# Performance work log

Hardware: AMD Instinct MI355X
Metric: run time of the kernel (lower is better)

The kernel has to match this reference:

```python
import jax, jax.numpy as jnp
import numpy as np

ALPHA = 0.2  # LeakyReLU negative slope


def setup_inputs() -> dict:
    key = jax.random.key(0)
    k1, k2, k3, k4 = jax.random.split(key, 4)
    B, N, in_dim, out_dim, n_heads = 4, 2048, 128, 32, 4
    H = jax.random.normal(k1, (B, N, in_dim), dtype=jnp.float32)
    adj = jax.random.randint(k2, (N, N), 0, 2).astype(jnp.float32)
    # xavier-uniform-like init for params
    limW = np.sqrt(6.0 / (in_dim + out_dim))
    W = jax.random.uniform(k3, (n_heads, in_dim, out_dim), minval=-limW, maxval=limW, dtype=jnp.float32)
    lima = np.sqrt(6.0 / (n_heads + 2 * out_dim))
    a = jax.random.uniform(k4, (n_heads, 2 * out_dim), minval=-lima, maxval=lima, dtype=jnp.float32)
    return {"H": H, "adj": adj, "W": W, "a": a}


def reference(H, adj, W, a):
    B, N, _ = H.shape
    n_heads, _, out_dim = W.shape
    # projected features: (B, H, N, F)
    Ht = jnp.einsum('bni,hio->bhno', H, W)
    # split attention vector: e_ij = leaky_relu(a_src . h_i + a_dst . h_j)
    a_src, a_dst = a[:, :out_dim], a[:, out_dim:]
    src = jnp.einsum('bhnf,hf->bhn', Ht, a_src)  # (B,H,N)
    dst = jnp.einsum('bhnf,hf->bhn', Ht, a_dst)  # (B,H,N)
    e = src[:, :, :, None] + dst[:, :, None, :]  # (B,H,N,N)
    e = jnp.where(e >= 0, e, ALPHA * e)          # leaky_relu
    mask = (adj + jnp.eye(N, dtype=adj.dtype)) != 0  # (N,N) bool, self-loops added
    e = jnp.where(mask[None, None], e, -jnp.inf)
    alpha = jax.nn.softmax(e, axis=-1)           # (B,H,N,N)
    H_new = jnp.einsum('bhnj,bhjf->bhnf', alpha, Ht)
    H_new = jnp.where(H_new > 0, H_new, jnp.expm1(H_new))  # ELU
    # concat heads: (B, N, n_heads*out_dim)
    H_new = jnp.transpose(H_new, (0, 2, 1, 3)).reshape(B, N, n_heads * out_dim)
    return H_new, alpha
```

## Files before the change

kernel.cpp:

```cpp
#include <hip/hip_runtime.h>
#include <hip/hip_bf16.h>
#include <math.h>


typedef float f32x4 __attribute__((ext_vector_type(4)));
typedef short bf16x8 __attribute__((ext_vector_type(8)));
typedef unsigned int u32;

#define LRELU 0.2f
#define LOG2E 1.44269504088896f
#define EXP2(x) __builtin_amdgcn_exp2f(x)

__device__ inline ushort f2b(float x) {
    unsigned int u = __float_as_uint(x);
    u += 0x7fffu + ((u >> 16) & 1u);
    return (ushort)(u >> 16);
}

__global__ __launch_bounds__(256) void k01(const float* __restrict__ adj,
                                           unsigned char* __restrict__ adjI,
                                           const float* __restrict__ H,
                                           const float* __restrict__ W,
                                           const float* __restrict__ a,
                                           __hip_bfloat16* __restrict__ HtT,
                                           float* __restrict__ src,
                                           float* __restrict__ dst) {
    __shared__ __align__(16) ushort Wbf[32 * 128];

    int bid = blockIdx.x;
    int t = threadIdx.x;

    if (bid >= 512) {
        int idx = (bid - 512) * 256 + t;
        int e0 = idx * 4;
        int row = e0 >> 11;
        int c0 = e0 & 2047;
        float4 v = *(const float4*)(adj + (size_t)e0);
        uchar4 o;
        o.x = (v.x != 0.f || c0     == row) ? 1 : 0;
        o.y = (v.y != 0.f || c0 + 1 == row) ? 1 : 0;
        o.z = (v.z != 0.f || c0 + 2 == row) ? 1 : 0;
        o.w = (v.w != 0.f || c0 + 3 == row) ? 1 : 0;
        *(uchar4*)(adjI + (size_t)e0) = o;
        return;
    }

    int ntile = bid & 31;
    int bh = bid >> 5;
    int b = bh >> 2, h = bh & 3;
    int lane = t & 63, w = t >> 6;
    int l15 = lane & 15, l4 = lane >> 4;

    #pragma unroll
    for (int u = 0; u < 16; ++u) {
        int idx = u * 256 + t;
        int i = idx >> 5, f = idx & 31;
        Wbf[(f * 128 + i) ^ ((f & 7) << 3)] = f2b(W[h * 4096 + idx]);
    }
    __syncthreads();

    int n = ntile * 64 + w * 16 + l15;
    const float* hrow = H + ((size_t)(b * 2048) + n) * 128;

    f32x4 acc0 = {0.f, 0.f, 0.f, 0.f};
    f32x4 acc1 = {0.f, 0.f, 0.f, 0.f};
    #pragma unroll
    for (int kc = 0; kc < 4; ++kc) {
        int k0 = kc * 32 + l4 * 8;
        float4 h0 = *(const float4*)(hrow + k0);
        float4 h1 = *(const float4*)(hrow + k0 + 4);
        union { u32 u[4]; bf16x8 v; } bu;
        asm("v_cvt_pk_bf16_f32 %0, %1, %2" : "=v"(bu.u[0]) : "v"(h0.x), "v"(h0.y));
        asm("v_cvt_pk_bf16_f32 %0, %1, %2" : "=v"(bu.u[1]) : "v"(h0.z), "v"(h0.w));
        asm("v_cvt_pk_bf16_f32 %0, %1, %2" : "=v"(bu.u[2]) : "v"(h1.x), "v"(h1.y));
        asm("v_cvt_pk_bf16_f32 %0, %1, %2" : "=v"(bu.u[3]) : "v"(h1.z), "v"(h1.w));
        bf16x8 bfrag = bu.v;
        bf16x8 af0 = *(const bf16x8*)&Wbf[(l15 * 128 + kc * 32 + l4 * 8) ^ ((l15 & 7) << 3)];
        bf16x8 af1 = *(const bf16x8*)&Wbf[((16 + l15) * 128 + kc * 32 + l4 * 8) ^ (((16 + l15) & 7) << 3)];
        acc0 = __builtin_amdgcn_mfma_f32_16x16x32_bf16(af0, bfrag, acc0, 0, 0, 0);
        acc1 = __builtin_amdgcn_mfma_f32_16x16x32_bf16(af1, bfrag, acc1, 0, 0, 0);
    }

    float sv = 0.f, dvv = 0.f;
    #pragma unroll
    for (int r = 0; r < 4; ++r) {
        int f0 = l4 * 4 + r;
        sv  += acc0[r] * a[h * 64 + f0]      + acc1[r] * a[h * 64 + 16 + f0];
        dvv += acc0[r] * a[h * 64 + 32 + f0] + acc1[r] * a[h * 64 + 48 + f0];
    }
    sv  += __shfl_xor(sv, 16);  sv  += __shfl_xor(sv, 32);
    dvv += __shfl_xor(dvv, 16); dvv += __shfl_xor(dvv, 32);
    if (l4 == 0) { src[bh * 2048 + n] = sv; dst[bh * 2048 + n] = dvv; }

    __syncthreads();
    ushort* T = Wbf;
    int nl = w * 16 + l15;
    #pragma unroll
    for (int r = 0; r < 4; ++r) {
        int f0 = l4 * 4 + r;
        T[f0 * 64 + nl]        = f2b(acc0[r]);
        T[(16 + f0) * 64 + nl] = f2b(acc1[r]);
    }
    __syncthreads();
    {
        int f = t >> 3, n8 = (t & 7) * 8;
        uint4 v = *(const uint4*)&T[f * 64 + n8];
        *(uint4*)((ushort*)HtT + (size_t)(bh * 32 + f) * 2048 + ntile * 64 + n8) = v;
    }
}

__global__ __launch_bounds__(256, 4) void k2_fused(const unsigned char* __restrict__ adjI,
                                                   const float* __restrict__ src,
                                                   const float* __restrict__ dst,
                                                   const __hip_bfloat16* __restrict__ HtT,
                                                   float* __restrict__ alpha,
                                                   float* __restrict__ outH) {
    __shared__ float dstS[2048];
    __shared__ float rowL[32], rowSrcS[32];
    __shared__ __align__(16) ushort As[2][32 * 128];

    int t = threadIdx.x;
    int mtile = blockIdx.x;
    int bh    = blockIdx.y;
    int lane = t & 63, w = t >> 6;
    int b = bh >> 2, h = bh & 3;
    int row0 = mtile * 32;

    const float4* dst4g = (const float4*)(dst + bh * 2048);
    #pragma unroll
    for (int u = 0; u < 2; ++u) {
        float4 v = dst4g[u * 256 + t];
        v.x *= LOG2E; v.y *= LOG2E; v.z *= LOG2E; v.w *= LOG2E;
        *(float4*)&dstS[(u * 256 + t) * 4] = v;
    }
    if (t < 32) rowSrcS[t] = src[bh * 2048 + row0 + t] * LOG2E;
    __syncthreads();

    for (int rr = 0; rr < 8; ++rr) {
        int r = w * 8 + rr;
        int gr = row0 + r;
        float sn = rowSrcS[r];
        const uint4* a16 = (const uint4*)(adjI + (size_t)gr * 2048);
        float S = 0.f;
        #pragma unroll
        for (int u = 0; u < 2; ++u) {
            uint4 ab = a16[u * 64 + lane];
            int jb = (u * 64 + lane) * 16;
            u32 words[4] = {ab.x, ab.y, ab.z, ab.w};
            #pragma unroll
            for (int wq = 0; wq < 4; ++wq) {
                float4 dv = *(const float4*)&dstS[jb + wq * 4];
                float dj[4] = {dv.x, dv.y, dv.z, dv.w};
                #pragma unroll
                for (int q = 0; q < 4; ++q) {
                    float ajf = (float)((words[wq] >> (8 * q)) & 0xffu);
                    float ee = sn + dj[q];
                    float vm = fmaxf(ee, LRELU * ee);
                    S = fmaf(EXP2(vm), ajf, S);
                }
            }
        }
        #pragma unroll
        for (int off = 32; off; off >>= 1) S += __shfl_xor(S, off);
        if (lane == 0) rowL[r] = -__log2f(S);
    }
    __syncthreads();

    f32x4 acc = {0.f, 0.f, 0.f, 0.f};
    int wr = w >> 1, wc = w & 1;
    int l15 = lane & 15, l4 = lane >> 4;
    int arow = wr * 16 + l15;
    const ushort* Bfp = (const ushort*)HtT + (size_t)(bh * 32 + wc * 16 + l15) * 2048 + l4 * 8;
    float* alphaRow = alpha + (size_t)(bh * 2048 + row0) * 2048;

    int sr = t >> 5;
    int sc4 = t & 31;

    float snR[4], LR[4];
    #pragma unroll
    for (int u = 0; u < 4; ++u) { snR[u] = rowSrcS[sr + u * 8]; LR[u] = rowL[sr + u * 8]; }

    auto loadA = [&](int k, u32* ar) {
        #pragma unroll
        for (int u = 0; u < 4; ++u)
            ar[u] = *(const u32*)(adjI + (size_t)(row0 + sr + u * 8) * 2048 + k * 128 + sc4 * 4);
    };
    auto loadB = [&](int k, bf16x8* br) {
        #pragma unroll
        for (int kk = 0; kk < 4; ++kk)
            br[kk] = *(const bf16x8*)(Bfp + (size_t)k * 128 + kk * 32);
    };
    auto stage = [&](int k, const u32* ar, ushort* Asb) {
        int jb = k * 128 + sc4 * 4;
        float4 dv = *(const float4*)&dstS[jb];
        float dj[4] = {dv.x, dv.y, dv.z, dv.w};
        #pragma unroll
        for (int u = 0; u < 4; ++u) {
            int r = sr + u * 8;
            float sn = snR[u], L = LR[u];
            u32 ab = ar[u];
            float o[4];
            #pragma unroll
            for (int q = 0; q < 4; ++q) {
                float ajf = (float)((ab >> (8 * q)) & 0xffu);
                float ee = sn + dj[q];
                float vm = fmaxf(ee + L, fmaf(ee, LRELU, L));
                o[q] = EXP2(vm) * ajf;
            }
            f32x4 ov = {o[0], o[1], o[2], o[3]};
            *(f32x4*)(alphaRow + (size_t)r * 2048 + jb) = ov;
            u32 lo, hi;
            asm("v_cvt_pk_bf16_f32 %0, %1, %2" : "=v"(lo) : "v"(o[0]), "v"(o[1]));
            asm("v_cvt_pk_bf16_f32 %0, %1, %2" : "=v"(hi) : "v"(o[2]), "v"(o[3]));
            uint2 pk = {lo, hi};
            *(uint2*)&Asb[(r * 128 + sc4 * 4) ^ ((r & 7) << 3)] = pk;
        }
    };
    auto mfmaPhase = [&](const bf16x8* br, const ushort* Asb) {
        #pragma unroll
        for (int kk = 0; kk < 4; ++kk) {
            bf16x8 af = *(const bf16x8*)&Asb[(arow * 128 + kk * 32 + l4 * 8) ^ ((arow & 7) << 3)];
            acc = __builtin_amdgcn_mfma_f32_16x16x32_bf16(af, br[kk], acc, 0, 0, 0);
        }
    };

    u32 aE[4], aO[4];
    bf16x8 bE[4], bO[4];
    loadA(0, aE); loadB(0, bE);

    for (int kp = 0; kp < 8; ++kp) {
        int ke = 2 * kp, ko = 2 * kp + 1;
        loadA(ko, aO); loadB(ko, bO);
        __builtin_amdgcn_sched_barrier(0);
        stage(ke, aE, As[0]);
        asm volatile("s_waitcnt lgkmcnt(0)" ::: "memory");
        __builtin_amdgcn_s_barrier();
        mfmaPhase(bE, As[0]);
        if (ko + 1 < 16) { loadA(ko + 1, aE); loadB(ko + 1, bE); }
        __builtin_amdgcn_sched_barrier(0);
        stage(ko, aO, As[1]);
        asm volatile("s_waitcnt lgkmcnt(0)" ::: "memory");
        __builtin_amdgcn_s_barrier();
        mfmaPhase(bO, As[1]);
    }

    #pragma unroll
    for (int q = 0; q < 4; ++q) {
        int node = row0 + wr * 16 + l4 * 4 + q;
        float v = acc[q];
        v = (v > 0.f) ? v : expm1f(v);
        outH[(size_t)(b * 2048 + node) * 128 + h * 32 + wc * 16 + l15] = v;
    }
}

extern "C" void kernel_launch(void* const* d_in, const int* in_sizes, int n_in,
                              void* d_out, int out_size, void* d_ws, size_t ws_size,
                              hipStream_t stream) {
    const float* H   = (const float*)d_in[0];
    const float* adj = (const float*)d_in[1];
    const float* W   = (const float*)d_in[2];
    const float* a   = (const float*)d_in[3];

    float* outH  = (float*)d_out;
    float* alpha = outH + (size_t)4 * 2048 * 128;

    char* ws = (char*)d_ws;
    __hip_bfloat16* HtT = (__hip_bfloat16*)ws;
    float* src = (float*)(ws + 2 * 1024 * 1024);
    float* dst = src + 32768;
    unsigned char* adjI = (unsigned char*)(ws + 2 * 1024 * 1024 + 256 * 1024);

    k01<<<4608, 256, 0, stream>>>(adj, adjI, H, W, a, HtT, src, dst);
    k2_fused<<<dim3(64, 16), 256, 0, stream>>>(adjI, src, dst, HtT, alpha, outH);
}
```

Baseline: 71.25 us.

## Stage half-row alpha tiles into large LDS buffer, cutting barriers per tile

The k2 main loop now works on two halves of 1024 columns instead of sixteen 128-column chunks. Each wave computes full 1024-wide alpha rows for its own 8 rows, writes them to global memory and to a 64KB bf16 LDS buffer, then syncs once before running all the MFMAs for that half. This is meant to cut the number of block barriers and to make the global alpha stores contiguous per row. In exchange, LDS use rises to roughly 72KB per block, so launch bounds drop from 4 to 2 blocks per CU and occupancy falls. Compute and MFMA phases also no longer overlap across chunks.

```diff
diff --git a/kernel.cpp b/kernel.cpp
--- a/kernel.cpp
+++ b/kernel.cpp
@@ -109,7 +109,7 @@
     }
 }
 
-__global__ __launch_bounds__(256, 4) void k2_fused(const unsigned char* __restrict__ adjI,
+__global__ __launch_bounds__(256, 2) void k2_fused(const unsigned char* __restrict__ adjI,
                                                    const float* __restrict__ src,
                                                    const float* __restrict__ dst,
                                                    const __hip_bfloat16* __restrict__ HtT,
@@ -117,7 +117,7 @@
                                                    float* __restrict__ outH) {
     __shared__ float dstS[2048];
     __shared__ float rowL[32], rowSrcS[32];
-    __shared__ __align__(16) ushort As[2][32 * 128];
+    __shared__ __align__(16) ushort As[32 * 1024];
 
     int t = threadIdx.x;
     int mtile = blockIdx.x;
@@ -173,75 +173,79 @@
     const ushort* Bfp = (const ushort*)HtT + (size_t)(bh * 32 + wc * 16 + l15) * 2048 + l4 * 8;
     float* alphaRow = alpha + (size_t)(bh * 2048 + row0) * 2048;
 
-    int sr = t >> 5;
-    int sc4 = t & 31;
-
-    float snR[4], LR[4];
-    #pragma unroll
-    for (int u = 0; u < 4; ++u) { snR[u] = rowSrcS[sr + u * 8]; LR[u] = rowL[sr + u * 8]; }
-
-    auto loadA = [&](int k, u32* ar) {
-        #pragma unroll
-        for (int u = 0; u < 4; ++u)
-            ar[u] = *(const u32*)(adjI + (size_t)(row0 + sr + u * 8) * 2048 + k * 128 + sc4 * 4);
-    };
-    auto loadB = [&](int k, bf16x8* br) {
+    #pragma unroll
+    for (int half = 0; half < 2; ++half) {
+        int c0 = half * 1024;
+
+        u32 abE[4], abO[4];
+        {
+            const u32* ap = (const u32*)(adjI + (size_t)(row0 + w * 8) * 2048 + c0);
+            #pragma unroll
+            for (int j = 0; j < 4; ++j) abE[j] = ap[j * 64 + lane];
+        }
+        #pragma unroll
+        for (int rr = 0; rr < 8; ++rr) {
+            int r = w * 8 + rr;
+            const u32* abC = (rr & 1) ? abO : abE;
+            u32*       abN = (rr & 1) ? abE : abO;
+            if (rr < 7) {
+                const u32* ap = (const u32*)(adjI + (size_t)(row0 + r + 1) * 2048 + c0);
+                #pragma unroll
+                for (int j = 0; j < 4; ++j) abN[j] = ap[j * 64 + lane];
+            }
+            __builtin_amdgcn_sched_barrier(0);
+            float sn = rowSrcS[r], L = rowL[r];
+            float* orow = alphaRow + (size_t)r * 2048 + c0;
+            #pragma unroll
+            for (int j = 0; j < 4; ++j) {
+                int col = j * 256 + lane * 4;
+                float4 dv = *(const float4*)&dstS[c0 + col];
+                float dj[4] = {dv.x, dv.y, dv.z, dv.w};
+                u32 ab = abC[j];
+                float o[4];
+                #pragma unroll
+                for (int q = 0; q < 4; ++q) {
+                    float ajf = (float)((ab >> (8 * q)) & 0xffu);
+                    float ee = sn + dj[q];
+                    float vm = fmaxf(ee + L, fmaf(ee, LRELU, L));
+                    o[q] = EXP2(vm) * ajf;
+                }
+                f32x4 ov = {o[0], o[1], o[2], o[3]};
+                *(f32x4*)(orow + col) = ov;
+                u32 lo, hi;
+                asm("v_cvt_pk_bf16_f32 %0, %1, %2" : "=v"(lo) : "v"(o[0]), "v"(o[1]));
+                asm("v_cvt_pk_bf16_f32 %0, %1, %2" : "=v"(hi) : "v"(o[2]), "v"(o[3]));
+                uint2 pk = {lo, hi};
+                *(uint2*)&As[(r * 1024 + col) ^ ((r & 7) << 3)] = pk;
+            }
+        }
+
+        bf16x8 bE[4], bO[4];
         #pragma unroll
         for (int kk = 0; kk < 4; ++kk)
-            br[kk] = *(const bf16x8*)(Bfp + (size_t)k * 128 + kk * 32);
-    };
-    auto stage = [&](int k, const u32* ar, ushort* Asb) {
-        int jb = k * 128 + sc4 * 4;
-        float4 dv = *(const float4*)&dstS[jb];
-        float dj[4] = {dv.x, dv.y, dv.z, dv.w};
-        #pragma unroll
-        for (int u = 0; u < 4; ++u) {
-            int r = sr + u * 8;
-            float sn = snR[u], L = LR[u];
-            u32 ab = ar[u];
-            float o[4];
-            #pragma unroll
-            for (int q = 0; q < 4; ++q) {
-                float ajf = (float)((ab >> (8 * q)) & 0xffu);
-                float ee = sn + dj[q];
-                float vm = fmaxf(ee + L, fmaf(ee, LRELU, L));
-                o[q] = EXP2(vm) * ajf;
-            }
-            f32x4 ov = {o[0], o[1], o[2], o[3]};
-            *(f32x4*)(alphaRow + (size_t)r * 2048 + jb) = ov;
-            u32 lo, hi;
-            asm("v_cvt_pk_bf16_f32 %0, %1, %2" : "=v"(lo) : "v"(o[0]), "v"(o[1]));
-            asm("v_cvt_pk_bf16_f32 %0, %1, %2" : "=v"(hi) : "v"(o[2]), "v"(o[3]));
-            uint2 pk = {lo, hi};
-            *(uint2*)&Asb[(r * 128 + sc4 * 4) ^ ((r & 7) << 3)] = pk;
-        }
-    };
-    auto mfmaPhase = [&](const bf16x8* br, const ushort* Asb) {
-        #pragma unroll
-        for (int kk = 0; kk < 4; ++kk) {
-            bf16x8 af = *(const bf16x8*)&Asb[(arow * 128 + kk * 32 + l4 * 8) ^ ((arow & 7) << 3)];
-            acc = __builtin_amdgcn_mfma_f32_16x16x32_bf16(af, br[kk], acc, 0, 0, 0);
-        }
-    };
-
-    u32 aE[4], aO[4];
-    bf16x8 bE[4], bO[4];
-    loadA(0, aE); loadB(0, bE);
-
-    for (int kp = 0; kp < 8; ++kp) {
-        int ke = 2 * kp, ko = 2 * kp + 1;
-        loadA(ko, aO); loadB(ko, bO);
-        __builtin_amdgcn_sched_barrier(0);
-        stage(ke, aE, As[0]);
+            bE[kk] = *(const bf16x8*)(Bfp + (size_t)(half * 8) * 128 + kk * 32);
         asm volatile("s_waitcnt lgkmcnt(0)" ::: "memory");
         __builtin_amdgcn_s_barrier();
-        mfmaPhase(bE, As[0]);
-        if (ko + 1 < 16) { loadA(ko + 1, aE); loadB(ko + 1, bE); }
-        __builtin_amdgcn_sched_barrier(0);
-        stage(ko, aO, As[1]);
+
+        #pragma unroll
+        for (int c = 0; c < 8; ++c) {
+            const bf16x8* bC = (c & 1) ? bO : bE;
+            bf16x8*       bN = (c & 1) ? bE : bO;
+            if (c < 7) {
+                #pragma unroll
+                for (int kk = 0; kk < 4; ++kk)
+                    bN[kk] = *(const bf16x8*)(Bfp + (size_t)(half * 8 + c + 1) * 128 + kk * 32);
+            }
+            __builtin_amdgcn_sched_barrier(0);
+            #pragma unroll
+            for (int kk = 0; kk < 4; ++kk) {
+                bf16x8 af = *(const bf16x8*)&As[(arow * 1024 + c * 128 + kk * 32 + l4 * 8) ^ ((arow & 7) << 3)];
+                acc = __builtin_amdgcn_mfma_f32_16x16x32_bf16(af, bC[kk], acc, 0, 0, 0);
+            }
+        }
+
         asm volatile("s_waitcnt lgkmcnt(0)" ::: "memory");
         __builtin_amdgcn_s_barrier();
-        mfmaPhase(bO, As[1]);
     }
 
     #pragma unroll
```

After: 84.34 us. +18.4%, slower.

## Restructure fused attention kernel to single-wave blocks of 16 rows without barriers

Applied to the files above, without the earlier changes.

The fused softmax/aggregation kernel moves from 256-thread blocks over 32 rows to 64-thread single-wavefront blocks over 16 rows, doubling the grid. With one wave per block, all __syncthreads and s_barrier calls are dropped. Each wave now computes both 16-column output halves with two MFMA accumulators and loads B fragments inline per chunk. This removes cross-wave synchronisation but reloads the 8KB dst vector into LDS per 16 rows (twice as often) and gives each wave more serial work and register pressure.

```diff
diff --git a/kernel.cpp b/kernel.cpp
--- a/kernel.cpp
+++ b/kernel.cpp
@@ -109,37 +109,36 @@
     }
 }
 
-__global__ __launch_bounds__(256, 4) void k2_fused(const unsigned char* __restrict__ adjI,
-                                                   const float* __restrict__ src,
-                                                   const float* __restrict__ dst,
-                                                   const __hip_bfloat16* __restrict__ HtT,
-                                                   float* __restrict__ alpha,
-                                                   float* __restrict__ outH) {
+__global__ __launch_bounds__(64, 2) void k2_fused(const unsigned char* __restrict__ adjI,
+                                                  const float* __restrict__ src,
+                                                  const float* __restrict__ dst,
+                                                  const __hip_bfloat16* __restrict__ HtT,
+                                                  float* __restrict__ alpha,
+                                                  float* __restrict__ outH) {
     __shared__ float dstS[2048];
-    __shared__ float rowL[32], rowSrcS[32];
-    __shared__ __align__(16) ushort As[2][32 * 128];
-
-    int t = threadIdx.x;
+    __shared__ float rowL[16], rowSrc[16];
+    __shared__ __align__(16) ushort As[2][16 * 128];
+
+    int lane = threadIdx.x;
     int mtile = blockIdx.x;
     int bh    = blockIdx.y;
-    int lane = t & 63, w = t >> 6;
     int b = bh >> 2, h = bh & 3;
-    int row0 = mtile * 32;
+    int row0 = mtile * 16;
+    int l15 = lane & 15, l4 = lane >> 4;
 
     const float4* dst4g = (const float4*)(dst + bh * 2048);
     #pragma unroll
-    for (int u = 0; u < 2; ++u) {
-        float4 v = dst4g[u * 256 + t];
+    for (int u = 0; u < 8; ++u) {
+        float4 v = dst4g[u * 64 + lane];
         v.x *= LOG2E; v.y *= LOG2E; v.z *= LOG2E; v.w *= LOG2E;
-        *(float4*)&dstS[(u * 256 + t) * 4] = v;
-    }
-    if (t < 32) rowSrcS[t] = src[bh * 2048 + row0 + t] * LOG2E;
-    __syncthreads();
-
-    for (int rr = 0; rr < 8; ++rr) {
-        int r = w * 8 + rr;
+        *(float4*)&dstS[(u * 64 + lane) * 4] = v;
+    }
+    if (lane < 16) rowSrc[lane] = src[bh * 2048 + row0 + lane] * LOG2E;
+
+    #pragma unroll
+    for (int r = 0; r < 16; ++r) {
         int gr = row0 + r;
-        float sn = rowSrcS[r];
+        float sn = rowSrc[r];
         const uint4* a16 = (const uint4*)(adjI + (size_t)gr * 2048);
         float S = 0.f;
         #pragma unroll
@@ -164,41 +163,33 @@
         for (int off = 32; off; off >>= 1) S += __shfl_xor(S, off);
         if (lane == 0) rowL[r] = -__log2f(S);
     }
-    __syncthreads();
-
-    f32x4 acc = {0.f, 0.f, 0.f, 0.f};
-    int wr = w >> 1, wc = w & 1;
-    int l15 = lane & 15, l4 = lane >> 4;
-    int arow = wr * 16 + l15;
-    const ushort* Bfp = (const ushort*)HtT + (size_t)(bh * 32 + wc * 16 + l15) * 2048 + l4 * 8;
+
+    int r2 = lane >> 5;
+    float snP[8], LP[8];
+    #pragma unroll
+    for (int p = 0; p < 8; ++p) { snP[p] = rowSrc[2 * p + r2]; LP[p] = rowL[2 * p + r2]; }
+
+    f32x4 acc0 = {0.f, 0.f, 0.f, 0.f};
+    f32x4 acc1 = {0.f, 0.f, 0.f, 0.f};
+    const ushort* Bf0 = (const ushort*)HtT + (size_t)(bh * 32 + l15) * 2048 + l4 * 8;
+    const ushort* Bf1 = (const ushort*)HtT + (size_t)(bh * 32 + 16 + l15) * 2048 + l4 * 8;
     float* alphaRow = alpha + (size_t)(bh * 2048 + row0) * 2048;
-
-    int sr = t >> 5;
-    int sc4 = t & 31;
-
-    float snR[4], LR[4];
-    #pragma unroll
-    for (int u = 0; u < 4; ++u) { snR[u] = rowSrcS[sr + u * 8]; LR[u] = rowL[sr + u * 8]; }
+    int sc = (lane & 31) * 4;
 
     auto loadA = [&](int k, u32* ar) {
         #pragma unroll
-        for (int u = 0; u < 4; ++u)
-            ar[u] = *(const u32*)(adjI + (size_t)(row0 + sr + u * 8) * 2048 + k * 128 + sc4 * 4);
-    };
-    auto loadB = [&](int k, bf16x8* br) {
-        #pragma unroll
-        for (int kk = 0; kk < 4; ++kk)
-            br[kk] = *(const bf16x8*)(Bfp + (size_t)k * 128 + kk * 32);
+        for (int p = 0; p < 8; ++p)
+            ar[p] = *(const u32*)(adjI + (size_t)(row0 + 2 * p + r2) * 2048 + k * 128 + sc);
     };
     auto stage = [&](int k, const u32* ar, ushort* Asb) {
-        int jb = k * 128 + sc4 * 4;
+        int jb = k * 128 + sc;
         float4 dv = *(const float4*)&dstS[jb];
         float dj[4] = {dv.x, dv.y, dv.z, dv.w};
         #pragma unroll
-        for (int u = 0; u < 4; ++u) {
-            int r = sr + u * 8;
-            float sn = snR[u], L = LR[u];
-            u32 ab = ar[u];
+        for (int p = 0; p < 8; ++p) {
+            int r = 2 * p + r2;
+            float sn = snP[p], L = LP[p];
+            u32 ab = ar[p];
             float o[4];
             #pragma unroll
             for (int q = 0; q < 4; ++q) {
@@ -213,43 +204,47 @@
             asm("v_cvt_pk_bf16_f32 %0, %1, %2" : "=v"(lo) : "v"(o[0]), "v"(o[1]));
             asm("v_cvt_pk_bf16_f32 %0, %1, %2" : "=v"(hi) : "v"(o[2]), "v"(o[3]));
             uint2 pk = {lo, hi};
-            *(uint2*)&Asb[(r * 128 + sc4 * 4) ^ ((r & 7) << 3)] = pk;
+            *(uint2*)&Asb[(r * 128 + sc) ^ ((r & 7) << 3)] = pk;
         }
     };
-    auto mfmaPhase = [&](const bf16x8* br, const ushort* Asb) {
+    auto chunk = [&](int k, const u32* aC, u32* aN, ushort* Asb) {
+        bf16x8 bf[8];
         #pragma unroll
         for (int kk = 0; kk < 4; ++kk) {
-            bf16x8 af = *(const bf16x8*)&Asb[(arow * 128 + kk * 32 + l4 * 8) ^ ((arow & 7) << 3)];
-            acc = __builtin_amdgcn_mfma_f32_16x16x32_bf16(af, br[kk], acc, 0, 0, 0);
+            bf[kk]     = *(const bf16x8*)(Bf0 + (size_t)k * 128 + kk * 32);
+            bf[4 + kk] = *(const bf16x8*)(Bf1 + (size_t)k * 128 + kk * 32);
+        }
+        if (k < 15) loadA(k + 1, aN);
+        __builtin_amdgcn_sched_barrier(0);
+        stage(k, aC, Asb);
+        bf16x8 af[4];
+        #pragma unroll
+        for (int kk = 0; kk < 4; ++kk)
+            af[kk] = *(const bf16x8*)&Asb[(l15 * 128 + kk * 32 + l4 * 8) ^ ((l15 & 7) << 3)];
+        #pragma unroll
+        for (int kk = 0; kk < 4; ++kk) {
+            acc0 = __builtin_amdgcn_mfma_f32_16x16x32_bf16(af[kk], bf[kk], acc0, 0, 0, 0);
+            acc1 = __builtin_amdgcn_mfma_f32_16x16x32_bf16(af[kk], bf[4 + kk], acc1, 0, 0, 0);
         }
     };
 
-    u32 aE[4], aO[4];
-    bf16x8 bE[4], bO[4];
-    loadA(0, aE); loadB(0, bE);
-
+    u32 aE[8], aO[8];
+    loadA(0, aE);
+    #pragma unroll
     for (int kp = 0; kp < 8; ++kp) {
-        int ke = 2 * kp, ko = 2 * kp + 1;
-        loadA(ko, aO); loadB(ko, bO);
-        __builtin_amdgcn_sched_barrier(0);
-        stage(ke, aE, As[0]);
-        asm volatile("s_waitcnt lgkmcnt(0)" ::: "memory");
-        __builtin_amdgcn_s_barrier();
-        mfmaPhase(bE, As[0]);
-        if (ko + 1 < 16) { loadA(ko + 1, aE); loadB(ko + 1, bE); }
-        __builtin_amdgcn_sched_barrier(0);
-        stage(ko, aO, As[1]);
-        asm volatile("s_waitcnt lgkmcnt(0)" ::: "memory");
-        __builtin_amdgcn_s_barrier();
-        mfmaPhase(bO, As[1]);
+        chunk(2 * kp,     aE, aO, As[0]);
+        chunk(2 * kp + 1, aO, aE, As[1]);
     }
 
     #pragma unroll
     for (int q = 0; q < 4; ++q) {
-        int node = row0 + wr * 16 + l4 * 4 + q;
-        float v = acc[q];
-        v = (v > 0.f) ? v : expm1f(v);
-        outH[(size_t)(b * 2048 + node) * 128 + h * 32 + wc * 16 + l15] = v;
+        int node = row0 + l4 * 4 + q;
+        float v0 = acc0[q];
+        v0 = (v0 > 0.f) ? v0 : expm1f(v0);
+        outH[(size_t)(b * 2048 + node) * 128 + h * 32 + l15] = v0;
+        float v1 = acc1[q];
+        v1 = (v1 > 0.f) ? v1 : expm1f(v1);
+        outH[(size_t)(b * 2048 + node) * 128 + h * 32 + 16 + l15] = v1;
     }
 }
 
@@ -271,5 +266,5 @@
     unsigned char* adjI = (unsigned char*)(ws + 2 * 1024 * 1024 + 256 * 1024);
 
     k01<<<4608, 256, 0, stream>>>(adj, adjI, H, W, a, HtT, src, dst);
-    k2_fused<<<dim3(64, 16), 256, 0, stream>>>(adjI, src, dst, HtT, alpha, outH);
-}
+    k2_fused<<<dim3(128, 16), 64, 0, stream>>>(adjI, src, dst, HtT, alpha, outH);
+}
```

Result: slower. 82.98 us (+16.5%).

## Split K across waves with register-resident alpha fragments feeding MFMA directly

Applied to the files above, without the earlier changes.

The fused attention kernel now handles 16 rows per block and splits the 2048-column reduction across four waves. Each lane computes alpha values straight into the MFMA A-fragment layout, so the LDS staging buffer and the per-chunk barriers go away. Partial accumulators are combined through LDS at the end. The adjacency mask becomes a float32 tensor instead of uint8, which removes the byte unpacking but makes the mask four times larger to write and read (16 MB versus 4 MB). The grid also doubles to 128x16 blocks.

```diff
diff --git a/kernel.cpp b/kernel.cpp
--- a/kernel.cpp
+++ b/kernel.cpp
@@ -18,7 +18,7 @@
 }
 
 __global__ __launch_bounds__(256) void k01(const float* __restrict__ adj,
-                                           unsigned char* __restrict__ adjI,
+                                           float* __restrict__ adjM,
                                            const float* __restrict__ H,
                                            const float* __restrict__ W,
                                            const float* __restrict__ a,
@@ -36,12 +36,12 @@
         int row = e0 >> 11;
         int c0 = e0 & 2047;
         float4 v = *(const float4*)(adj + (size_t)e0);
-        uchar4 o;
-        o.x = (v.x != 0.f || c0     == row) ? 1 : 0;
-        o.y = (v.y != 0.f || c0 + 1 == row) ? 1 : 0;
-        o.z = (v.z != 0.f || c0 + 2 == row) ? 1 : 0;
-        o.w = (v.w != 0.f || c0 + 3 == row) ? 1 : 0;
-        *(uchar4*)(adjI + (size_t)e0) = o;
+        f32x4 o;
+        o[0] = (v.x != 0.f || c0     == row) ? 1.f : 0.f;
+        o[1] = (v.y != 0.f || c0 + 1 == row) ? 1.f : 0.f;
+        o[2] = (v.z != 0.f || c0 + 2 == row) ? 1.f : 0.f;
+        o[3] = (v.w != 0.f || c0 + 3 == row) ? 1.f : 0.f;
+        *(f32x4*)(adjM + (size_t)e0) = o;
         return;
     }
 
@@ -109,22 +109,23 @@
     }
 }
 
-__global__ __launch_bounds__(256, 4) void k2_fused(const unsigned char* __restrict__ adjI,
+__global__ __launch_bounds__(256, 4) void k2_fused(const float* __restrict__ adjM,
                                                    const float* __restrict__ src,
                                                    const float* __restrict__ dst,
                                                    const __hip_bfloat16* __restrict__ HtT,
                                                    float* __restrict__ alpha,
                                                    float* __restrict__ outH) {
     __shared__ float dstS[2048];
-    __shared__ float rowL[32], rowSrcS[32];
-    __shared__ __align__(16) ushort As[2][32 * 128];
+    __shared__ float Scomb[4][16];
+    __shared__ float AccComb[3 * 528];
 
     int t = threadIdx.x;
+    int lane = t & 63, ks = t >> 6;
     int mtile = blockIdx.x;
     int bh    = blockIdx.y;
-    int lane = t & 63, w = t >> 6;
     int b = bh >> 2, h = bh & 3;
-    int row0 = mtile * 32;
+    int row0 = mtile * 16;
+    int l15 = lane & 15, l4 = lane >> 4;
 
     const float4* dst4g = (const float4*)(dst + bh * 2048);
     #pragma unroll
@@ -133,123 +134,125 @@
         v.x *= LOG2E; v.y *= LOG2E; v.z *= LOG2E; v.w *= LOG2E;
         *(float4*)&dstS[(u * 256 + t) * 4] = v;
     }
-    if (t < 32) rowSrcS[t] = src[bh * 2048 + row0 + t] * LOG2E;
-    __syncthreads();
-
-    for (int rr = 0; rr < 8; ++rr) {
-        int r = w * 8 + rr;
-        int gr = row0 + r;
-        float sn = rowSrcS[r];
-        const uint4* a16 = (const uint4*)(adjI + (size_t)gr * 2048);
-        float S = 0.f;
-        #pragma unroll
-        for (int u = 0; u < 2; ++u) {
-            uint4 ab = a16[u * 64 + lane];
-            int jb = (u * 64 + lane) * 16;
-            u32 words[4] = {ab.x, ab.y, ab.z, ab.w};
+    asm volatile("s_waitcnt lgkmcnt(0)" ::: "memory");
+    __builtin_amdgcn_s_barrier();
+
+    int gr = row0 + l15;
+    float sn = src[bh * 2048 + gr] * LOG2E;
+    const float* amRow = adjM + (size_t)gr * 2048;
+
+    float S = 0.f;
+    for (int c = 0; c < 16; ++c) {
+        int k0 = ks * 512 + c * 32 + l4 * 8;
+        float4 a0 = *(const float4*)(amRow + k0);
+        float4 a1 = *(const float4*)(amRow + k0 + 4);
+        float4 d0 = *(const float4*)&dstS[k0];
+        float4 d1 = *(const float4*)&dstS[k0 + 4];
+        float am[8] = {a0.x, a0.y, a0.z, a0.w, a1.x, a1.y, a1.z, a1.w};
+        float dj[8] = {d0.x, d0.y, d0.z, d0.w, d1.x, d1.y, d1.z, d1.w};
+        #pragma unroll
+        for (int i = 0; i < 8; ++i) {
+            float ee = sn + dj[i];
+            float vm = fmaxf(ee, LRELU * ee);
+            S = fmaf(EXP2(vm), am[i], S);
+        }
+    }
+    S += __shfl_xor(S, 16);
+    S += __shfl_xor(S, 32);
+    if (l4 == 0) Scomb[ks][l15] = S;
+    asm volatile("s_waitcnt lgkmcnt(0)" ::: "memory");
+    __builtin_amdgcn_s_barrier();
+
+    float Sf = (Scomb[0][l15] + Scomb[1][l15]) + (Scomb[2][l15] + Scomb[3][l15]);
+    float L = -__log2f(Sf);
+    float snL = sn + L;
+    float L08 = 0.8f * L;
+
+    f32x4 acc0 = {0.f, 0.f, 0.f, 0.f};
+    f32x4 acc1 = {0.f, 0.f, 0.f, 0.f};
+    const ushort* Bp0 = (const ushort*)HtT + (size_t)(bh * 32 + l15) * 2048;
+    const ushort* Bp1 = (const ushort*)HtT + (size_t)(bh * 32 + 16 + l15) * 2048;
+    float* aRow = alpha + (size_t)(bh * 2048 + gr) * 2048;
+
+    float amE[8], amO[8];
+    bf16x8 bE0, bE1, bO0, bO1;
+
+    auto loadAM = [&](int c, float* am) {
+        int k0 = ks * 512 + c * 32 + l4 * 8;
+        float4 a0 = *(const float4*)(amRow + k0);
+        float4 a1 = *(const float4*)(amRow + k0 + 4);
+        am[0] = a0.x; am[1] = a0.y; am[2] = a0.z; am[3] = a0.w;
+        am[4] = a1.x; am[5] = a1.y; am[6] = a1.z; am[7] = a1.w;
+    };
+    auto loadB2 = [&](int c, bf16x8& b0, bf16x8& b1) {
+        int k0 = ks * 512 + c * 32 + l4 * 8;
+        b0 = *(const bf16x8*)(Bp0 + k0);
+        b1 = *(const bf16x8*)(Bp1 + k0);
+    };
+    auto chunkB = [&](int c, const float* am, bf16x8 b0, bf16x8 b1) {
+        int k0 = ks * 512 + c * 32 + l4 * 8;
+        float4 d0 = *(const float4*)&dstS[k0];
+        float4 d1 = *(const float4*)&dstS[k0 + 4];
+        float dj[8] = {d0.x, d0.y, d0.z, d0.w, d1.x, d1.y, d1.z, d1.w};
+        float o[8];
+        #pragma unroll
+        for (int i = 0; i < 8; ++i) {
+            float eeL = snL + dj[i];
+            float tt = fmaf(eeL, LRELU, L08);
+            float vm = fmaxf(eeL, tt);
+            o[i] = EXP2(vm) * am[i];
+        }
+        f32x4 ov0 = {o[0], o[1], o[2], o[3]};
+        f32x4 ov1 = {o[4], o[5], o[6], o[7]};
+        *(f32x4*)(aRow + k0) = ov0;
+        *(f32x4*)(aRow + k0 + 4) = ov1;
+        union { u32 u[4]; bf16x8 v; } au;
+        asm("v_cvt_pk_bf16_f32 %0, %1, %2" : "=v"(au.u[0]) : "v"(o[0]), "v"(o[1]));
+        asm("v_cvt_pk_bf16_f32 %0, %1, %2" : "=v"(au.u[1]) : "v"(o[2]), "v"(o[3]));
+        asm("v_cvt_pk_bf16_f32 %0, %1, %2" : "=v"(au.u[2]) : "v"(o[4]), "v"(o[5]));
+        asm("v_cvt_pk_bf16_f32 %0, %1, %2" : "=v"(au.u[3]) : "v"(o[6]), "v"(o[7]));
+        acc0 = __builtin_amdgcn_mfma_f32_16x16x32_bf16(au.v, b0, acc0, 0, 0, 0);
+        acc1 = __builtin_amdgcn_mfma_f32_16x16x32_bf16(au.v, b1, acc1, 0, 0, 0);
+    };
+
+    loadAM(0, amE); loadB2(0, bE0, bE1);
+    #pragma unroll
+    for (int cp = 0; cp < 8; ++cp) {
+        int ce = 2 * cp, co = ce + 1;
+        loadAM(co, amO); loadB2(co, bO0, bO1);
+        __builtin_amdgcn_sched_barrier(0);
+        chunkB(ce, amE, bE0, bE1);
+        if (co < 15) { loadAM(co + 1, amE); loadB2(co + 1, bE0, bE1); }
+        __builtin_amdgcn_sched_barrier(0);
+        chunkB(co, amO, bO0, bO1);
+    }
+
+    if (ks != 0) {
+        #pragma unroll
+        for (int q = 0; q < 4; ++q) {
+            int row = l4 * 4 + q;
+            AccComb[(ks - 1) * 528 + row * 33 + l15]      = acc0[q];
+            AccComb[(ks - 1) * 528 + row * 33 + 16 + l15] = acc1[q];
+        }
+    }
+    asm volatile("s_waitcnt lgkmcnt(0)" ::: "memory");
+    __builtin_amdgcn_s_barrier();
+    if (ks == 0) {
+        #pragma unroll
+        for (int q = 0; q < 4; ++q) {
+            int row = l4 * 4 + q;
+            float v0 = acc0[q], v1 = acc1[q];
             #pragma unroll
-            for (int wq = 0; wq < 4; ++wq) {
-                float4 dv = *(const float4*)&dstS[jb + wq * 4];
-                float dj[4] = {dv.x, dv.y, dv.z, dv.w};
-                #pragma unroll
-                for (int q = 0; q < 4; ++q) {
-                    float ajf = (float)((words[wq] >> (8 * q)) & 0xffu);
-                    float ee = sn + dj[q];
-                    float vm = fmaxf(ee, LRELU * ee);
-                    S = fmaf(EXP2(vm), ajf, S);
-                }
+            for (int j = 0; j < 3; ++j) {
+                v0 += AccComb[j * 528 + row * 33 + l15];
+                v1 += AccComb[j * 528 + row * 33 + 16 + l15];
             }
-        }
-        #pragma unroll
-        for (int off = 32; off; off >>= 1) S += __shfl_xor(S, off);
-        if (lane == 0) rowL[r] = -__log2f(S);
-    }
-    __syncthreads();
-
-    f32x4 acc = {0.f, 0.f, 0.f, 0.f};
-    int wr = w >> 1, wc = w & 1;
-    int l15 = lane & 15, l4 = lane >> 4;
-    int arow = wr * 16 + l15;
-    const ushort* Bfp = (const ushort*)HtT + (size_t)(bh * 32 + wc * 16 + l15) * 2048 + l4 * 8;
-    float* alphaRow = alpha + (size_t)(bh * 2048 + row0) * 2048;
-
-    int sr = t >> 5;
-    int sc4 = t & 31;
-
-    float snR[4], LR[4];
-    #pragma unroll
-    for (int u = 0; u < 4; ++u) { snR[u] = rowSrcS[sr + u * 8]; LR[u] = rowL[sr + u * 8]; }
-
-    auto loadA = [&](int k, u32* ar) {
-        #pragma unroll
-        for (int u = 0; u < 4; ++u)
-            ar[u] = *(const u32*)(adjI + (size_t)(row0 + sr + u * 8) * 2048 + k * 128 + sc4 * 4);
-    };
-    auto loadB = [&](int k, bf16x8* br) {
-        #pragma unroll
-        for (int kk = 0; kk < 4; ++kk)
-            br[kk] = *(const bf16x8*)(Bfp + (size_t)k * 128 + kk * 32);
-    };
-    auto stage = [&](int k, const u32* ar, ushort* Asb) {
-        int jb = k * 128 + sc4 * 4;
-        float4 dv = *(const float4*)&dstS[jb];
-        float dj[4] = {dv.x, dv.y, dv.z, dv.w};
-        #pragma unroll
-        for (int u = 0; u < 4; ++u) {
-            int r = sr + u * 8;
-            float sn = snR[u], L = LR[u];
-            u32 ab = ar[u];
-            float o[4];
-            #pragma unroll
-            for (int q = 0; q < 4; ++q) {
-                float ajf = (float)((ab >> (8 * q)) & 0xffu);
-                float ee = sn + dj[q];
-                float vm = fmaxf(ee + L, fmaf(ee, LRELU, L));
-                o[q] = EXP2(vm) * ajf;
-            }
-            f32x4 ov = {o[0], o[1], o[2], o[3]};
-            *(f32x4*)(alphaRow + (size_t)r * 2048 + jb) = ov;
-            u32 lo, hi;
-            asm("v_cvt_pk_bf16_f32 %0, %1, %2" : "=v"(lo) : "v"(o[0]), "v"(o[1]));
-            asm("v_cvt_pk_bf16_f32 %0, %1, %2" : "=v"(hi) : "v"(o[2]), "v"(o[3]));
-            uint2 pk = {lo, hi};
-            *(uint2*)&Asb[(r * 128 + sc4 * 4) ^ ((r & 7) << 3)] = pk;
-        }
-    };
-    auto mfmaPhase = [&](const bf16x8* br, const ushort* Asb) {
-        #pragma unroll
-        for (int kk = 0; kk < 4; ++kk) {
-            bf16x8 af = *(const bf16x8*)&Asb[(arow * 128 + kk * 32 + l4 * 8) ^ ((arow & 7) << 3)];
-            acc = __builtin_amdgcn_mfma_f32_16x16x32_bf16(af, br[kk], acc, 0, 0, 0);
-        }
-    };
-
-    u32 aE[4], aO[4];
-    bf16x8 bE[4], bO[4];
-    loadA(0, aE); loadB(0, bE);
-
-    for (int kp = 0; kp < 8; ++kp) {
-        int ke = 2 * kp, ko = 2 * kp + 1;
-        loadA(ko, aO); loadB(ko, bO);
-        __builtin_amdgcn_sched_barrier(0);
-        stage(ke, aE, As[0]);
-        asm volatile("s_waitcnt lgkmcnt(0)" ::: "memory");
-        __builtin_amdgcn_s_barrier();
-        mfmaPhase(bE, As[0]);
-        if (ko + 1 < 16) { loadA(ko + 1, aE); loadB(ko + 1, bE); }
-        __builtin_amdgcn_sched_barrier(0);
-        stage(ko, aO, As[1]);
-        asm volatile("s_waitcnt lgkmcnt(0)" ::: "memory");
-        __builtin_amdgcn_s_barrier();
-        mfmaPhase(bO, As[1]);
-    }
-
-    #pragma unroll
-    for (int q = 0; q < 4; ++q) {
-        int node = row0 + wr * 16 + l4 * 4 + q;
-        float v = acc[q];
-        v = (v > 0.f) ? v : expm1f(v);
-        outH[(size_t)(b * 2048 + node) * 128 + h * 32 + wc * 16 + l15] = v;
+            v0 = (v0 > 0.f) ? v0 : expm1f(v0);
+            v1 = (v1 > 0.f) ? v1 : expm1f(v1);
+            size_t base = (size_t)(b * 2048 + row0 + row) * 128 + h * 32;
+            outH[base + l15]      = v0;
+            outH[base + 16 + l15] = v1;
+        }
     }
 }
 
@@ -266,10 +269,10 @@
 
     char* ws = (char*)d_ws;
     __hip_bfloat16* HtT = (__hip_bfloat16*)ws;
-    float* src = (float*)(ws + 2 * 1024 * 1024);
-    float* dst = src + 32768;
-    unsigned char* adjI = (unsigned char*)(ws + 2 * 1024 * 1024 + 256 * 1024);
-
-    k01<<<4608, 256, 0, stream>>>(adj, adjI, H, W, a, HtT, src, dst);
-    k2_fused<<<dim3(64, 16), 256, 0, stream>>>(adjI, src, dst, HtT, alpha, outH);
-}
+    float* src  = (float*)(ws + 2 * 1024 * 1024);
+    float* dst  = src + 32768;
+    float* adjM = (float*)(ws + 2 * 1024 * 1024 + 256 * 1024);
+
+    k01<<<4608, 256, 0, stream>>>(adj, adjM, H, W, a, HtT, src, dst);
+    k2_fused<<<dim3(128, 16), 256, 0, stream>>>(adjM, src, dst, HtT, alpha, outH);
+}
```

Result: slower. 125.3 us (+75.9%).
